# Kernel tuning notes

Hardware: AMD Instinct MI355X
Metric: run time of the kernel (lower is better)

## Reference

```python
import jax, jax.numpy as jnp
from jax import lax
import numpy as np

S, B, T = 512, 256, 128


def setup_inputs() -> dict:
    key = jax.random.key(0)
    k1, k2, k3, k4 = jax.random.split(key, 4)
    emissions = jax.random.normal(k1, (S, B, T), dtype=jnp.float32)
    mask = jnp.ones((S, B), dtype=jnp.int32)  # all positions valid
    start_transitions = jax.random.normal(k2, (T,), dtype=jnp.float32)
    end_transitions = jax.random.normal(k3, (T,), dtype=jnp.float32)
    transitions = jax.random.normal(k4, (T, T), dtype=jnp.float32)
    return {
        "emissions": emissions,
        "mask": mask,
        "start_transitions": start_transitions,
        "end_transitions": end_transitions,
        "transitions": transitions,
    }


def reference(emissions, mask, start_transitions, end_transitions, transitions):
    """Viterbi decode. emissions: [S,B,T], mask: [S,B].
    Returns (best_tags [B,S] int32, best_path_score [B] float32)."""
    seq_len, batch, num_tags = emissions.shape
    maskb = mask.astype(bool)

    score0 = start_transitions[None, :] + emissions[0]  # [B,T]

    def fwd_step(score, inp):
        em_t, m_t = inp  # [B,T], [B]
        # [B, T_prev, T_next]
        ns = score[:, :, None] + transitions[None, :, :] + em_t[:, None, :]
        next_score = ns.max(axis=1)          # [B,T]
        idx = ns.argmax(axis=1)              # [B,T] best previous tag
        score = jnp.where(m_t[:, None], next_score, score)
        return score, idx

    final_score, history = lax.scan(fwd_step, score0, (emissions[1:], maskb[1:]))
    final_score = final_score + end_transitions[None, :]

    best_last = jnp.argmax(final_score, axis=1)   # [B] tag at last valid position
    best_score = jnp.max(final_score, axis=1)     # [B]

    barange = jnp.arange(batch)

    def back_step(tag, inp):
        hist_t, m_t = inp  # [B,T], [B]
        prev = hist_t[barange, tag]
        tag = jnp.where(m_t, prev, tag)  # only follow history inside the sequence
        return tag, tag

    # reverse scan over transitions t -> t+1 for t = S-2 .. 0; ys[t] = tag at time t
    _, tags_prefix = lax.scan(back_step, best_last, (history, maskb[1:]), reverse=True)
    tags = jnp.concatenate([tags_prefix, best_last[None, :]], axis=0)  # [S,B]
    return tags.T.astype(jnp.int32), best_score
```

## Files before the change

kernel.cpp:

```cpp
#include <hip/hip_runtime.h>

#define SLEN  512
#define BATCH 256
#define NTAGS 128
#define NTHR  1024

__device__ __forceinline__ int dpp_qperm_b1(int x) {
    return __builtin_amdgcn_update_dpp(0, x, 0xB1, 0xF, 0xF, true);
}
__device__ __forceinline__ int dpp_qperm_4e(int x) {
    return __builtin_amdgcn_update_dpp(0, x, 0x4E, 0xF, 0xF, true);
}
__device__ __forceinline__ int swz_xor4(int x) {
    return __builtin_amdgcn_ds_swizzle(x, 0x101F);
}

struct VI { float v; int i; };
__device__ __forceinline__ VI vmax2(VI a, VI b) { return (b.v > a.v) ? b : a; }

__global__ __launch_bounds__(NTHR, 4) void viterbi_kernel(
    const float* __restrict__ em,
    const int*   __restrict__ mask,
    const float* __restrict__ start_t,
    const float* __restrict__ end_t,
    const float* __restrict__ trans,
    float* __restrict__ out)
{
    const int b    = blockIdx.x;
    const int tid  = threadIdx.x;
    const int j    = tid >> 3;
    const int h    = tid & 7;
    const int base = h << 4;
    const bool writer = (h == 0);
    const int jslot = j + (j >> 4) * 4;

    __shared__ __align__(16) float scbuf[2][8 * 20];
    __shared__ float fin[NTAGS];
    __shared__ int   maskv[SLEN];
    __shared__ unsigned char hist[SLEN - 1][NTAGS];
    __shared__ unsigned char exitc[8][NTAGS];
    __shared__ unsigned char st_tags[8];
    __shared__ unsigned char tagseq[SLEN];
    __shared__ float bestval_s;
    __shared__ int   bestj_s;

    const float* trp = trans + (size_t)base * NTAGS + j;
    const float t00 = trp[ 0*NTAGS], t01 = trp[ 1*NTAGS], t02 = trp[ 2*NTAGS], t03 = trp[ 3*NTAGS];
    const float t04 = trp[ 4*NTAGS], t05 = trp[ 5*NTAGS], t06 = trp[ 6*NTAGS], t07 = trp[ 7*NTAGS];
    const float t08 = trp[ 8*NTAGS], t09 = trp[ 9*NTAGS], t10 = trp[10*NTAGS], t11 = trp[11*NTAGS];
    const float t12 = trp[12*NTAGS], t13 = trp[13*NTAGS], t14 = trp[14*NTAGS], t15 = trp[15*NTAGS];

    if (tid < SLEN)
        maskv[tid] = mask[tid * BATCH + b];

    float scj = 0.f;
    if (writer) {
        scj = start_t[j] + em[(size_t)b * NTAGS + j];
        scbuf[0][jslot] = scj;
    }
    __syncthreads();

    const float* emp = em + (size_t)BATCH * NTAGS + (size_t)b * NTAGS + j;
    float em_next = *emp;

    int p = 0;
    for (int t = 1; t < SLEN; ++t) {
        const float em_cur = em_next;
        if (t + 1 < SLEN) { emp += BATCH * NTAGS; em_next = *emp; }

        const float4* sq = (const float4*)&scbuf[p][h * 20];
        const float4 q0 = sq[0], q1 = sq[1], q2 = sq[2], q3 = sq[3];

        const float c00 = (q0.x + t00) + em_cur, c01 = (q0.y + t01) + em_cur;
        const float c02 = (q0.z + t02) + em_cur, c03 = (q0.w + t03) + em_cur;
        const float c04 = (q1.x + t04) + em_cur, c05 = (q1.y + t05) + em_cur;
        const float c06 = (q1.z + t06) + em_cur, c07 = (q1.w + t07) + em_cur;
        const float c08 = (q2.x + t08) + em_cur, c09 = (q2.y + t09) + em_cur;
        const float c10 = (q2.z + t10) + em_cur, c11 = (q2.w + t11) + em_cur;
        const float c12 = (q3.x + t12) + em_cur, c13 = (q3.y + t13) + em_cur;
        const float c14 = (q3.z + t14) + em_cur, c15 = (q3.w + t15) + em_cur;

        const VI m0 = vmax2(VI{c00, 0}, VI{c01, 1}),  m1 = vmax2(VI{c02, 2}, VI{c03, 3});
        const VI m2 = vmax2(VI{c04, 4}, VI{c05, 5}),  m3 = vmax2(VI{c06, 6}, VI{c07, 7});
        const VI m4 = vmax2(VI{c08, 8}, VI{c09, 9}),  m5 = vmax2(VI{c10,10}, VI{c11,11});
        const VI m6 = vmax2(VI{c12,12}, VI{c13,13}),  m7 = vmax2(VI{c14,14}, VI{c15,15});
        const VI n0 = vmax2(m0, m1), n1 = vmax2(m2, m3);
        const VI n2 = vmax2(m4, m5), n3 = vmax2(m6, m7);
        const VI o0 = vmax2(n0, n1), o1 = vmax2(n2, n3);
        const VI r  = vmax2(o0, o1);

        float v  = r.v;
        int   gi = base + r.i;
        {
            float vo = __int_as_float(dpp_qperm_b1(__float_as_int(v)));
            int   io = dpp_qperm_b1(gi);
            if (vo > v) { v = vo; gi = io; }
        }
        {
            float vo = __int_as_float(dpp_qperm_4e(__float_as_int(v)));
            int   io = dpp_qperm_4e(gi);
            if (vo > v) { v = vo; gi = io; }
        }
        {
            float vo = __int_as_float(swz_xor4(__float_as_int(v)));
            int   io = swz_xor4(gi);
            if (vo > v) { v = vo; gi = io; }
        }

        if (writer) {
            hist[t - 1][j] = (unsigned char)gi;
            scj = maskv[t] ? v : scj;
            scbuf[p ^ 1][jslot] = scj;
        }
        __syncthreads();
        p ^= 1;
    }

    if (writer) fin[j] = scj + end_t[j];
    __syncthreads();

    if (tid < 64) {
        float v  = fin[tid]; int bj = tid;
        float v1 = fin[tid + 64];
        if (v1 > v) { v = v1; bj = tid + 64; }
#pragma unroll
        for (int off = 32; off > 0; off >>= 1) {
            float ov = __shfl_xor(v, off, 64);
            int   oj = __shfl_xor(bj, off, 64);
            if (ov > v || (ov == v && oj < bj)) { v = ov; bj = oj; }
        }
        if (tid == 0) { bestval_s = v; bestj_s = bj; }
    }
    __syncthreads();

    {
        const int k = tid & 127;
        const int c = tid >> 7;
        int tag = k;
        for (int u = 63; u >= 0; --u) {
            const int s = c * 64 + u;
            if (s <= SLEN - 2) {
                int pv = hist[s][tag];
                tag = maskv[s + 1] ? pv : tag;
            }
        }
        exitc[c][k] = (unsigned char)tag;
    }
    __syncthreads();

    if (tid == 0) {
        int tag = bestj_s;
        for (int c = 7; c >= 0; --c) {
            st_tags[c] = (unsigned char)tag;
            tag = exitc[c][tag];
        }
        out[BATCH * SLEN + b] = bestval_s;
    }
    __syncthreads();

    if (tid < 8) {
        const int c = tid;
        int tag = st_tags[c];
        if (c == 7) tagseq[SLEN - 1] = (unsigned char)tag;
        const int shi = (c == 7) ? (SLEN - 2) : (c * 64 + 63);
        for (int s = shi; s >= c * 64; --s) {
            int pv = hist[s][tag];
            tag = maskv[s + 1] ? pv : tag;
            tagseq[s] = (unsigned char)tag;
        }
    }
    __syncthreads();

    if (tid < SLEN)
        out[b * SLEN + tid] = (float)tagseq[tid];
}

extern "C" void kernel_launch(void* const* d_in, const int* in_sizes, int n_in,
                              void* d_out, int out_size, void* d_ws, size_t ws_size,
                              hipStream_t stream) {
    const float* em      = (const float*)d_in[0];
    const int*   mask    = (const int*)d_in[1];
    const float* start_t = (const float*)d_in[2];
    const float* end_t   = (const float*)d_in[3];
    const float* trans   = (const float*)d_in[4];
    float* out = (float*)d_out;

    viterbi_kernel<<<dim3(BATCH), dim3(NTHR), 0, stream>>>(
        em, mask, start_t, end_t, trans, out);
}
```

Before: 406.0 us.

## Replace value-index argmax with packed max then masked-min index recovery

The per-step argmax over 16 candidates per thread and across 8 lanes no longer carries value/index pairs through compare-select chains. It first computes the max with packed f32 adds, v_max3 and DPP/swizzle fmax. It then recovers the argmax index as the min of (c-M)*(-1e12)+k using packed FMA and v_min3. The __syncthreads is also replaced with an explicit lgkmcnt wait plus s_barrier. This relies on exact float equality and large-scale arithmetic for ties, and may pick a different index when near-equal values round, and it doubles the arithmetic passes.

```diff
diff --git a/kernel.cpp b/kernel.cpp
--- a/kernel.cpp
+++ b/kernel.cpp
@@ -1,4 +1,5 @@
 #include <hip/hip_runtime.h>
+#include <stdint.h>
 
 #define SLEN  512
 #define BATCH 256
@@ -15,8 +16,36 @@
     return __builtin_amdgcn_ds_swizzle(x, 0x101F);
 }
 
-struct VI { float v; int i; };
-__device__ __forceinline__ VI vmax2(VI a, VI b) { return (b.v > a.v) ? b : a; }
+__device__ __forceinline__ float combine_max8(float v) {
+    float vo = __int_as_float(dpp_qperm_b1(__float_as_int(v))); v = fmaxf(v, vo);
+    vo = __int_as_float(dpp_qperm_4e(__float_as_int(v)));       v = fmaxf(v, vo);
+    vo = __int_as_float(swz_xor4(__float_as_int(v)));           v = fmaxf(v, vo);
+    return v;
+}
+__device__ __forceinline__ float combine_min8(float v) {
+    float vo = __int_as_float(dpp_qperm_b1(__float_as_int(v))); v = fminf(v, vo);
+    vo = __int_as_float(dpp_qperm_4e(__float_as_int(v)));       v = fminf(v, vo);
+    vo = __int_as_float(swz_xor4(__float_as_int(v)));           v = fminf(v, vo);
+    return v;
+}
+
+__device__ __forceinline__ uint64_t pk2(float lo, float hi) {
+    union { float f[2]; uint64_t u; } x; x.f[0] = lo; x.f[1] = hi; return x.u;
+}
+__device__ __forceinline__ float pklo(uint64_t a) { return __uint_as_float((unsigned)a); }
+__device__ __forceinline__ float pkhi(uint64_t a) { return __uint_as_float((unsigned)(a >> 32)); }
+__device__ __forceinline__ uint64_t pk_add(uint64_t a, uint64_t b) {
+    uint64_t d; asm("v_pk_add_f32 %0, %1, %2" : "=v"(d) : "v"(a), "v"(b)); return d;
+}
+__device__ __forceinline__ uint64_t pk_fma(uint64_t a, uint64_t b, uint64_t c) {
+    uint64_t d; asm("v_pk_fma_f32 %0, %1, %2, %3" : "=v"(d) : "v"(a), "v"(b), "v"(c)); return d;
+}
+__device__ __forceinline__ float max3(float a, float b, float c) {
+    float d; asm("v_max3_f32 %0, %1, %2, %3" : "=v"(d) : "v"(a), "v"(b), "v"(c)); return d;
+}
+__device__ __forceinline__ float min3(float a, float b, float c) {
+    float d; asm("v_min3_f32 %0, %1, %2, %3" : "=v"(d) : "v"(a), "v"(b), "v"(c)); return d;
+}
 
 __global__ __launch_bounds__(NTHR, 4) void viterbi_kernel(
     const float* __restrict__ em,
@@ -45,10 +74,24 @@
     __shared__ int   bestj_s;
 
     const float* trp = trans + (size_t)base * NTAGS + j;
-    const float t00 = trp[ 0*NTAGS], t01 = trp[ 1*NTAGS], t02 = trp[ 2*NTAGS], t03 = trp[ 3*NTAGS];
-    const float t04 = trp[ 4*NTAGS], t05 = trp[ 5*NTAGS], t06 = trp[ 6*NTAGS], t07 = trp[ 7*NTAGS];
-    const float t08 = trp[ 8*NTAGS], t09 = trp[ 9*NTAGS], t10 = trp[10*NTAGS], t11 = trp[11*NTAGS];
-    const float t12 = trp[12*NTAGS], t13 = trp[13*NTAGS], t14 = trp[14*NTAGS], t15 = trp[15*NTAGS];
+    const uint64_t trP0 = pk2(trp[ 0*NTAGS], trp[ 1*NTAGS]);
+    const uint64_t trP1 = pk2(trp[ 2*NTAGS], trp[ 3*NTAGS]);
+    const uint64_t trP2 = pk2(trp[ 4*NTAGS], trp[ 5*NTAGS]);
+    const uint64_t trP3 = pk2(trp[ 6*NTAGS], trp[ 7*NTAGS]);
+    const uint64_t trP4 = pk2(trp[ 8*NTAGS], trp[ 9*NTAGS]);
+    const uint64_t trP5 = pk2(trp[10*NTAGS], trp[11*NTAGS]);
+    const uint64_t trP6 = pk2(trp[12*NTAGS], trp[13*NTAGS]);
+    const uint64_t trP7 = pk2(trp[14*NTAGS], trp[15*NTAGS]);
+
+    const uint64_t kP0 = pk2((float)(base +  0), (float)(base +  1));
+    const uint64_t kP1 = pk2((float)(base +  2), (float)(base +  3));
+    const uint64_t kP2 = pk2((float)(base +  4), (float)(base +  5));
+    const uint64_t kP3 = pk2((float)(base +  6), (float)(base +  7));
+    const uint64_t kP4 = pk2((float)(base +  8), (float)(base +  9));
+    const uint64_t kP5 = pk2((float)(base + 10), (float)(base + 11));
+    const uint64_t kP6 = pk2((float)(base + 12), (float)(base + 13));
+    const uint64_t kP7 = pk2((float)(base + 14), (float)(base + 15));
+    const uint64_t negH = pk2(-1e12f, -1e12f);
 
     if (tid < SLEN)
         maskv[tid] = mask[tid * BATCH + b];
@@ -71,48 +114,51 @@
         const float4* sq = (const float4*)&scbuf[p][h * 20];
         const float4 q0 = sq[0], q1 = sq[1], q2 = sq[2], q3 = sq[3];
 
-        const float c00 = (q0.x + t00) + em_cur, c01 = (q0.y + t01) + em_cur;
-        const float c02 = (q0.z + t02) + em_cur, c03 = (q0.w + t03) + em_cur;
-        const float c04 = (q1.x + t04) + em_cur, c05 = (q1.y + t05) + em_cur;
-        const float c06 = (q1.z + t06) + em_cur, c07 = (q1.w + t07) + em_cur;
-        const float c08 = (q2.x + t08) + em_cur, c09 = (q2.y + t09) + em_cur;
-        const float c10 = (q2.z + t10) + em_cur, c11 = (q2.w + t11) + em_cur;
-        const float c12 = (q3.x + t12) + em_cur, c13 = (q3.y + t13) + em_cur;
-        const float c14 = (q3.z + t14) + em_cur, c15 = (q3.w + t15) + em_cur;
-
-        const VI m0 = vmax2(VI{c00, 0}, VI{c01, 1}),  m1 = vmax2(VI{c02, 2}, VI{c03, 3});
-        const VI m2 = vmax2(VI{c04, 4}, VI{c05, 5}),  m3 = vmax2(VI{c06, 6}, VI{c07, 7});
-        const VI m4 = vmax2(VI{c08, 8}, VI{c09, 9}),  m5 = vmax2(VI{c10,10}, VI{c11,11});
-        const VI m6 = vmax2(VI{c12,12}, VI{c13,13}),  m7 = vmax2(VI{c14,14}, VI{c15,15});
-        const VI n0 = vmax2(m0, m1), n1 = vmax2(m2, m3);
-        const VI n2 = vmax2(m4, m5), n3 = vmax2(m6, m7);
-        const VI o0 = vmax2(n0, n1), o1 = vmax2(n2, n3);
-        const VI r  = vmax2(o0, o1);
-
-        float v  = r.v;
-        int   gi = base + r.i;
-        {
-            float vo = __int_as_float(dpp_qperm_b1(__float_as_int(v)));
-            int   io = dpp_qperm_b1(gi);
-            if (vo > v) { v = vo; gi = io; }
-        }
-        {
-            float vo = __int_as_float(dpp_qperm_4e(__float_as_int(v)));
-            int   io = dpp_qperm_4e(gi);
-            if (vo > v) { v = vo; gi = io; }
-        }
-        {
-            float vo = __int_as_float(swz_xor4(__float_as_int(v)));
-            int   io = swz_xor4(gi);
-            if (vo > v) { v = vo; gi = io; }
-        }
+        const uint64_t emP = pk2(em_cur, em_cur);
+        const uint64_t c0 = pk_add(pk_add(pk2(q0.x, q0.y), trP0), emP);
+        const uint64_t c1 = pk_add(pk_add(pk2(q0.z, q0.w), trP1), emP);
+        const uint64_t c2 = pk_add(pk_add(pk2(q1.x, q1.y), trP2), emP);
+        const uint64_t c3 = pk_add(pk_add(pk2(q1.z, q1.w), trP3), emP);
+        const uint64_t c4 = pk_add(pk_add(pk2(q2.x, q2.y), trP4), emP);
+        const uint64_t c5 = pk_add(pk_add(pk2(q2.z, q2.w), trP5), emP);
+        const uint64_t c6 = pk_add(pk_add(pk2(q3.x, q3.y), trP6), emP);
+        const uint64_t c7 = pk_add(pk_add(pk2(q3.z, q3.w), trP7), emP);
+
+        const float x0 = max3(pklo(c0), pkhi(c0), pklo(c1));
+        const float x1 = max3(pkhi(c1), pklo(c2), pkhi(c2));
+        const float x2 = max3(pklo(c3), pkhi(c3), pklo(c4));
+        const float x3 = max3(pkhi(c4), pklo(c5), pkhi(c5));
+        const float x4 = max3(pklo(c6), pkhi(c6), pklo(c7));
+        const float x5 = pkhi(c7);
+        const float y0 = max3(x0, x1, x2);
+        const float y1 = max3(x3, x4, x5);
+        const float M  = combine_max8(fmaxf(y0, y1));
+
+        const uint64_t negMP = pk2(-M, -M);
+        const uint64_t v0 = pk_fma(pk_add(c0, negMP), negH, kP0);
+        const uint64_t v1 = pk_fma(pk_add(c1, negMP), negH, kP1);
+        const uint64_t v2 = pk_fma(pk_add(c2, negMP), negH, kP2);
+        const uint64_t v3 = pk_fma(pk_add(c3, negMP), negH, kP3);
+        const uint64_t v4 = pk_fma(pk_add(c4, negMP), negH, kP4);
+        const uint64_t v5 = pk_fma(pk_add(c5, negMP), negH, kP5);
+        const uint64_t v6 = pk_fma(pk_add(c6, negMP), negH, kP6);
+        const uint64_t v7 = pk_fma(pk_add(c7, negMP), negH, kP7);
+        const float z0 = min3(pklo(v0), pkhi(v0), pklo(v1));
+        const float z1 = min3(pkhi(v1), pklo(v2), pkhi(v2));
+        const float z2 = min3(pklo(v3), pkhi(v3), pklo(v4));
+        const float z3 = min3(pkhi(v4), pklo(v5), pkhi(v5));
+        const float z4 = min3(pklo(v6), pkhi(v6), pklo(v7));
+        const float z5 = pkhi(v7);
+        const float u0 = min3(z0, z1, z2);
+        const float u1 = min3(z3, z4, z5);
+        const float vmin = combine_min8(fminf(u0, u1));
 
         if (writer) {
-            hist[t - 1][j] = (unsigned char)gi;
-            scj = maskv[t] ? v : scj;
+            hist[t - 1][j] = (unsigned char)(int)vmin;
+            scj = maskv[t] ? M : scj;
             scbuf[p ^ 1][jslot] = scj;
         }
-        __syncthreads();
+        asm volatile("s_waitcnt lgkmcnt(0)\n\ts_barrier" ::: "memory");
         p ^= 1;
     }
 
```

Result: slower. 419.5 us (+3.3%).

## Replace value-index argmax with max3 reduction plus min-index recovery

Applied to the files above, without the earlier changes.

The paired value/index argmax tree is replaced by a value-only max reduction using v_max3_f32 and DPP cross-lane max. A second pass recovers the smallest index attaining the max through an fma that scales each score's distance from the max by a large negative constant, then a min3 tree and DPP min. The ds_swizzle step becomes a DPP row half-mirror, and __syncthreads is replaced with an inline s_waitcnt plus s_barrier. This trades dependent select chains for more ALU ops, but index recovery is exact only when score gaps times 1e12 dominate the tag index, and the half-mirror shuffle must match the old xor-4 pairing.

```diff
diff --git a/kernel.cpp b/kernel.cpp
--- a/kernel.cpp
+++ b/kernel.cpp
@@ -11,12 +11,29 @@
 __device__ __forceinline__ int dpp_qperm_4e(int x) {
     return __builtin_amdgcn_update_dpp(0, x, 0x4E, 0xF, 0xF, true);
 }
-__device__ __forceinline__ int swz_xor4(int x) {
-    return __builtin_amdgcn_ds_swizzle(x, 0x101F);
-}
-
-struct VI { float v; int i; };
-__device__ __forceinline__ VI vmax2(VI a, VI b) { return (b.v > a.v) ? b : a; }
+__device__ __forceinline__ int dpp_hmirror(int x) {
+    return __builtin_amdgcn_update_dpp(0, x, 0x141, 0xF, 0xF, true);
+}
+
+__device__ __forceinline__ float combine_max8(float v) {
+    float vo = __int_as_float(dpp_qperm_b1(__float_as_int(v))); v = fmaxf(v, vo);
+    vo = __int_as_float(dpp_qperm_4e(__float_as_int(v)));       v = fmaxf(v, vo);
+    vo = __int_as_float(dpp_hmirror(__float_as_int(v)));        v = fmaxf(v, vo);
+    return v;
+}
+__device__ __forceinline__ float combine_min8(float v) {
+    float vo = __int_as_float(dpp_qperm_b1(__float_as_int(v))); v = fminf(v, vo);
+    vo = __int_as_float(dpp_qperm_4e(__float_as_int(v)));       v = fminf(v, vo);
+    vo = __int_as_float(dpp_hmirror(__float_as_int(v)));        v = fminf(v, vo);
+    return v;
+}
+
+__device__ __forceinline__ float max3(float a, float b, float c) {
+    float d; asm("v_max3_f32 %0, %1, %2, %3" : "=v"(d) : "v"(a), "v"(b), "v"(c)); return d;
+}
+__device__ __forceinline__ float min3(float a, float b, float c) {
+    float d; asm("v_min3_f32 %0, %1, %2, %3" : "=v"(d) : "v"(a), "v"(b), "v"(c)); return d;
+}
 
 __global__ __launch_bounds__(NTHR, 4) void viterbi_kernel(
     const float* __restrict__ em,
@@ -50,6 +67,16 @@
     const float t08 = trp[ 8*NTAGS], t09 = trp[ 9*NTAGS], t10 = trp[10*NTAGS], t11 = trp[11*NTAGS];
     const float t12 = trp[12*NTAGS], t13 = trp[13*NTAGS], t14 = trp[14*NTAGS], t15 = trp[15*NTAGS];
 
+    const float k00 = (float)(base +  0), k01 = (float)(base +  1);
+    const float k02 = (float)(base +  2), k03 = (float)(base +  3);
+    const float k04 = (float)(base +  4), k05 = (float)(base +  5);
+    const float k06 = (float)(base +  6), k07 = (float)(base +  7);
+    const float k08 = (float)(base +  8), k09 = (float)(base +  9);
+    const float k10 = (float)(base + 10), k11 = (float)(base + 11);
+    const float k12 = (float)(base + 12), k13 = (float)(base + 13);
+    const float k14 = (float)(base + 14), k15 = (float)(base + 15);
+    const float NH = -1e12f;
+
     if (tid < SLEN)
         maskv[tid] = mask[tid * BATCH + b];
 
@@ -80,39 +107,38 @@
         const float c12 = (q3.x + t12) + em_cur, c13 = (q3.y + t13) + em_cur;
         const float c14 = (q3.z + t14) + em_cur, c15 = (q3.w + t15) + em_cur;
 
-        const VI m0 = vmax2(VI{c00, 0}, VI{c01, 1}),  m1 = vmax2(VI{c02, 2}, VI{c03, 3});
-        const VI m2 = vmax2(VI{c04, 4}, VI{c05, 5}),  m3 = vmax2(VI{c06, 6}, VI{c07, 7});
-        const VI m4 = vmax2(VI{c08, 8}, VI{c09, 9}),  m5 = vmax2(VI{c10,10}, VI{c11,11});
-        const VI m6 = vmax2(VI{c12,12}, VI{c13,13}),  m7 = vmax2(VI{c14,14}, VI{c15,15});
-        const VI n0 = vmax2(m0, m1), n1 = vmax2(m2, m3);
-        const VI n2 = vmax2(m4, m5), n3 = vmax2(m6, m7);
-        const VI o0 = vmax2(n0, n1), o1 = vmax2(n2, n3);
-        const VI r  = vmax2(o0, o1);
-
-        float v  = r.v;
-        int   gi = base + r.i;
-        {
-            float vo = __int_as_float(dpp_qperm_b1(__float_as_int(v)));
-            int   io = dpp_qperm_b1(gi);
-            if (vo > v) { v = vo; gi = io; }
-        }
-        {
-            float vo = __int_as_float(dpp_qperm_4e(__float_as_int(v)));
-            int   io = dpp_qperm_4e(gi);
-            if (vo > v) { v = vo; gi = io; }
-        }
-        {
-            float vo = __int_as_float(swz_xor4(__float_as_int(v)));
-            int   io = swz_xor4(gi);
-            if (vo > v) { v = vo; gi = io; }
-        }
+        const float x0 = max3(c00, c01, c02);
+        const float x1 = max3(c03, c04, c05);
+        const float x2 = max3(c06, c07, c08);
+        const float x3 = max3(c09, c10, c11);
+        const float x4 = max3(c12, c13, c14);
+        const float y0 = max3(x0, x1, x2);
+        const float y1 = max3(x3, x4, c15);
+        const float M  = combine_max8(fmaxf(y0, y1));
+
+        const float v00 = fmaf(c00 - M, NH, k00), v01 = fmaf(c01 - M, NH, k01);
+        const float v02 = fmaf(c02 - M, NH, k02), v03 = fmaf(c03 - M, NH, k03);
+        const float v04 = fmaf(c04 - M, NH, k04), v05 = fmaf(c05 - M, NH, k05);
+        const float v06 = fmaf(c06 - M, NH, k06), v07 = fmaf(c07 - M, NH, k07);
+        const float v08 = fmaf(c08 - M, NH, k08), v09 = fmaf(c09 - M, NH, k09);
+        const float v10 = fmaf(c10 - M, NH, k10), v11 = fmaf(c11 - M, NH, k11);
+        const float v12 = fmaf(c12 - M, NH, k12), v13 = fmaf(c13 - M, NH, k13);
+        const float v14 = fmaf(c14 - M, NH, k14), v15 = fmaf(c15 - M, NH, k15);
+        const float z0 = min3(v00, v01, v02);
+        const float z1 = min3(v03, v04, v05);
+        const float z2 = min3(v06, v07, v08);
+        const float z3 = min3(v09, v10, v11);
+        const float z4 = min3(v12, v13, v14);
+        const float u0 = min3(z0, z1, z2);
+        const float u1 = min3(z3, z4, v15);
+        const float vmin = combine_min8(fminf(u0, u1));
 
         if (writer) {
-            hist[t - 1][j] = (unsigned char)gi;
-            scj = maskv[t] ? v : scj;
+            hist[t - 1][j] = (unsigned char)(int)vmin;
+            scj = maskv[t] ? M : scj;
             scbuf[p ^ 1][jslot] = scj;
         }
-        __syncthreads();
+        asm volatile("s_waitcnt lgkmcnt(0)\n\ts_barrier" ::: "memory");
         p ^= 1;
     }
 
```

Measured after the change: 389.5 us. 1.04x faster.
